# Kernel optimization log

Hardware: AMD Instinct MI355X
Metric: run time of the kernel (lower is better)

The kernel has to match this reference:

```python
import jax, jax.numpy as jnp
import numpy as np

B, T, D, H, TW = 4, 2048, 2048, 8, 4
DH = D // H


def setup_inputs() -> dict:
    key = jax.random.key(0)
    ks = jax.random.split(key, 16)
    s = lambda k, shape, std: jax.random.normal(k, shape, dtype=jnp.float32) * std
    inp = {
        "x": jax.random.normal(ks[0], (B, T, D), dtype=jnp.float32),
        "segment_pos": jnp.tile(jnp.arange(T, dtype=jnp.int32), (B, 1)),
        # linear_y / linear_x: width -> lru_width, std = 1/sqrt(width)
        "Wy": s(ks[1], (D, D), (1.0 / D) ** 0.5),
        "by": jnp.zeros((D,), jnp.float32),
        "Wx": s(ks[2], (D, D), (1.0 / D) ** 0.5),
        "bx": jnp.zeros((D,), jnp.float32),
        # depthwise causal conv: [temporal_width, lru_width]
        "conv_w": s(ks[3], (TW, D), (1.0 / TW) ** 0.5),
        "conv_b": jnp.zeros((D,), jnp.float32),
        # RG-LRU block-diagonal gates: [H, D/H, D/H]
        "gx_w": s(ks[4], (H, DH, DH), (1.0 / DH) ** 0.5),
        "gx_b": jnp.zeros((H, DH), jnp.float32),
        "ga_w": s(ks[5], (H, DH, DH), (1.0 / DH) ** 0.5),
        "ga_b": jnp.zeros((H, DH), jnp.float32),
        # a_param: softplus(a_param) > 0 controls decay rate
        "a_param": jnp.log(jnp.exp(jax.random.uniform(ks[6], (D,), minval=0.3, maxval=0.9)) - 1.0 + 1e-6),
        # linear_out: lru_width -> width, std = 1/sqrt(lru_width)
        "Wout": s(ks[7], (D, D), (1.0 / D) ** 0.5),
        "bout": jnp.zeros((D,), jnp.float32),
    }
    return inp


def _causal_conv1d(x, w, b, segment_pos):
    # depthwise causal conv over time; contributions from other segments masked
    t = x.shape[1]
    acc = jnp.zeros_like(x)
    for i in range(TW):
        shift = TW - 1 - i  # input at t - shift, weighted by w[i]
        xs = x if shift == 0 else jnp.pad(x, ((0, 0), (shift, 0), (0, 0)))[:, :t]
        mask = (segment_pos >= shift)[..., None].astype(x.dtype)
        acc = acc + xs * mask * w[i]
    return acc + b


def _rg_lru(x, segment_pos, gx_w, gx_b, ga_w, ga_b, a_param):
    b, t, d = x.shape
    xr = x.reshape(b, t, H, DH)
    gate_x = jax.nn.sigmoid(jnp.einsum("bthi,hij->bthj", xr, gx_w) + gx_b).reshape(b, t, d)
    gate_a = jax.nn.sigmoid(jnp.einsum("bthi,hij->bthj", xr, ga_w) + ga_b).reshape(b, t, d)
    log_a = -8.0 * gate_a * jax.nn.softplus(a_param)  # [B,T,D]
    a = jnp.exp(log_a)
    reset = (segment_pos == 0)[..., None]  # [B,T,1]
    multiplier = jnp.sqrt(jnp.maximum(1.0 - jnp.exp(2.0 * log_a), 0.0))
    multiplier = jnp.where(reset, 1.0, multiplier)
    normed = x * gate_x * multiplier
    a_scan = jnp.where(reset, 0.0, a)

    def step(h, inputs):
        a_t, x_t = inputs
        h = a_t * h + x_t
        return h, h

    h0 = jnp.zeros((b, d), x.dtype)
    _, ys = jax.lax.scan(step, h0, (a_scan.transpose(1, 0, 2), normed.transpose(1, 0, 2)))
    return ys.transpose(1, 0, 2)


def reference(x, segment_pos, Wy, by, Wx, bx, conv_w, conv_b, gx_w, gx_b, ga_w, ga_b, a_param, Wout, bout):
    y = jax.nn.gelu(x @ Wy.T + by, approximate=True)
    x_proj = x @ Wx.T + bx
    x_conv = _causal_conv1d(x_proj, conv_w, conv_b, segment_pos)
    x_lru = _rg_lru(x_conv, segment_pos, gx_w, gx_b, ga_w, ga_b, a_param)
    out = (x_lru * y) @ Wout.T + bout
    return out
```

## Files before the change

kernel.cpp:

```cpp
#include <hip/hip_runtime.h>
#include <cstdint>
#include <cstddef>

typedef __bf16 bf16;
typedef __bf16 bf16x8 __attribute__((ext_vector_type(8)));
typedef __bf16 bf16x4 __attribute__((ext_vector_type(4)));
typedef float f32x4 __attribute__((ext_vector_type(4)));

#define BDIM 4
#define TDIM 2048
#define DDIM 2048
#define HDIM 8
#define DHD 256
#define MTOT 8192
#define NCHUNK 64
#define LCHUNK 32

__device__ __forceinline__ void stage16(const bf16* g, bf16* l) {
  __builtin_amdgcn_global_load_lds(
      (const __attribute__((address_space(1))) void*)g,
      (__attribute__((address_space(3))) void*)l, 16, 0, 0);
}

#define BARX() __builtin_amdgcn_s_barrier()
#define SCHB() __builtin_amdgcn_sched_barrier(0)
#define WAITVM(N) asm volatile("s_waitcnt vmcnt(" #N ")")

__device__ __forceinline__ float sigmoid_f(float x) {
  return __fdividef(1.f, 1.f + __expf(-x));
}
__device__ __forceinline__ float gelu_tanh(float v) {
  float u = 0.7978845608028654f * (v + 0.044715f * v * v * v);
  u = fminf(fmaxf(u, -15.f), 15.f);
  float t = __expf(2.f * u);
  return 0.5f * v * (1.f + __fdividef(t - 1.f, t + 1.f));
}
__device__ __forceinline__ float softplus_f(float x) {
  return __logf(1.f + __expf(x));
}

__global__ __launch_bounds__(256) void f2b(const float* __restrict__ src,
                                           bf16* __restrict__ dst) {
  size_t i = ((size_t)blockIdx.x * 256 + threadIdx.x) * 8;
  const float4 a = *(const float4*)(src + i);
  const float4 b = *(const float4*)(src + i + 4);
  bf16x8 r;
  r[0] = (bf16)a.x; r[1] = (bf16)a.y; r[2] = (bf16)a.z; r[3] = (bf16)a.w;
  r[4] = (bf16)b.x; r[5] = (bf16)b.y; r[6] = (bf16)b.z; r[7] = (bf16)b.w;
  *(bf16x8*)(dst + i) = r;
}

__global__ __launch_bounds__(256) void f2b2(const float* __restrict__ s0,
                                            const float* __restrict__ s1,
                                            bf16* __restrict__ d0,
                                            bf16* __restrict__ d1) {
  const float* src = blockIdx.y ? s1 : s0;
  bf16* dst = blockIdx.y ? d1 : d0;
  size_t i = ((size_t)blockIdx.x * 256 + threadIdx.x) * 8;
  const float4 a = *(const float4*)(src + i);
  const float4 b = *(const float4*)(src + i + 4);
  bf16x8 r;
  r[0] = (bf16)a.x; r[1] = (bf16)a.y; r[2] = (bf16)a.z; r[3] = (bf16)a.w;
  r[4] = (bf16)b.x; r[5] = (bf16)b.y; r[6] = (bf16)b.z; r[7] = (bf16)b.w;
  *(bf16x8*)(dst + i) = r;
}

template <typename TO, int EPI>
__global__ __launch_bounds__(512, 2) void gemm256(
    const bf16* __restrict__ A, const bf16* __restrict__ Bm,
    const float* __restrict__ bias, TO* __restrict__ C,
    int K, int lda, int ldb, int ldc) {
  const int gx = gridDim.x, gy = gridDim.y;
  const int nwg = gx * gy;
  const int did = blockIdx.x + gx * blockIdx.y;
  const int cpx = nwg >> 3;
  const int lid = (did & 7) * cpx + (did >> 3);
  const int n0 = (lid % gx) * 256;
  const int m0 = (lid / gx) * 256;

  __shared__ bf16 sA0[256 * 64];
  __shared__ bf16 sA1[256 * 64];
  __shared__ bf16 sB0[256 * 64];
  __shared__ bf16 sB1[256 * 64];
  const int tid = threadIdx.x;
  const int lane = tid & 63;
  const int wid = tid >> 6;
  const int wr = wid >> 2;
  const int wc = wid & 3;
  const int quad = lane >> 4;
  const int l15 = lane & 15;

  const int sr = tid >> 3;
  const int ks8 = ((tid & 7) ^ (sr & 7)) << 3;
  const bf16* Ag = A + (size_t)(m0 + sr) * lda + ks8;
  const bf16* Bg = Bm + (size_t)(n0 + sr) * ldb + ks8;

  const int swz0 = ((quad) ^ (l15 & 7)) << 3;
  const int swz1 = ((4 + quad) ^ (l15 & 7)) << 3;

  f32x4 acc[8][4];
#pragma unroll
  for (int i = 0; i < 8; ++i)
#pragma unroll
    for (int j = 0; j < 4; ++j)
#pragma unroll
      for (int r = 0; r < 4; ++r) acc[i][j][r] = 0.f;

  const int NT = K >> 6;

#define STG_A(ARR, H, TK)                                                     \
  do {                                                                        \
    _Pragma("unroll") for (int j_ = 0; j_ < 2; ++j_) {                        \
      const int c_ = (H) * 2 + j_;                                            \
      stage16(Ag + (size_t)(c_ * 64) * lda + (size_t)(TK) * 64,               \
              &ARR[(c_ * 64 + wid * 8) * 64]);                                \
    }                                                                         \
  } while (0)
#define STG_B(ARR, H, TK)                                                     \
  do {                                                                        \
    _Pragma("unroll") for (int j_ = 0; j_ < 2; ++j_) {                        \
      const int c_ = (H) * 2 + j_;                                            \
      stage16(Bg + (size_t)(c_ * 64) * ldb + (size_t)(TK) * 64,               \
              &ARR[(c_ * 64 + wid * 8) * 64]);                                \
    }                                                                         \
  } while (0)

  bf16x8 aq0[4][2], aq1[4][2], b0[2][2], b1[2][2];

#define RDA(DST, MH, ARR)                                                     \
  do {                                                                        \
    _Pragma("unroll") for (int mi_ = 0; mi_ < 4; ++mi_) {                     \
      const int arow_ = wr * 128 + (MH) * 64 + mi_ * 16 + l15;                \
      DST[mi_][0] = *(const bf16x8*)(&ARR[arow_ * 64] + swz0);                \
      DST[mi_][1] = *(const bf16x8*)(&ARR[arow_ * 64] + swz1);                \
    }                                                                         \
  } while (0)
#define RDB(DST, NH, ARR)                                                     \
  do {                                                                        \
    _Pragma("unroll") for (int ni_ = 0; ni_ < 2; ++ni_) {                     \
      const int brow_ = wc * 64 + (NH) * 32 + ni_ * 16 + l15;                 \
      DST[ni_][0] = *(const bf16x8*)(&ARR[brow_ * 64] + swz0);                \
      DST[ni_][1] = *(const bf16x8*)(&ARR[brow_ * 64] + swz1);                \
    }                                                                         \
  } while (0)
#define MFMAQ(MH, NH, AA, BB)                                                 \
  do {                                                                        \
    __builtin_amdgcn_s_setprio(1);                                            \
    _Pragma("unroll") for (int mi_ = 0; mi_ < 4; ++mi_)                       \
        _Pragma("unroll") for (int ni_ = 0; ni_ < 2; ++ni_) {                 \
      acc[(MH)*4 + mi_][(NH)*2 + ni_] = __builtin_amdgcn_mfma_f32_16x16x32_bf16( \
          AA[mi_][0], BB[ni_][0], acc[(MH)*4 + mi_][(NH)*2 + ni_], 0, 0, 0);  \
      acc[(MH)*4 + mi_][(NH)*2 + ni_] = __builtin_amdgcn_mfma_f32_16x16x32_bf16( \
          AA[mi_][1], BB[ni_][1], acc[(MH)*4 + mi_][(NH)*2 + ni_], 0, 0, 0);  \
    }                                                                         \
    __builtin_amdgcn_s_setprio(0);                                            \
  } while (0)

#define TILE(SAs, SBs, SAo, SBo, T)                                           \
  do {                                                                        \
    const int tn_ = ((T) + 1 < NT) ? (T) + 1 : NT - 1;                        \
    const int tnn_ = ((T) + 2 < NT) ? (T) + 2 : NT - 1;                       \
                                                                     \
    WAITVM(4);                                                                \
    SCHB();                                                                   \
    STG_B(SBo, 1, tn_);                                                       \
    RDB(b1, 1, SBs);                                                          \
    MFMAQ(0, 0, aq0, b0);                                                     \
    BARX();                                                                   \
                                                                     \
    STG_A(SAo, 1, tn_);                                                       \
    RDA(aq1, 1, SAs);                                                         \
    MFMAQ(0, 1, aq0, b1);                                                     \
    BARX();                                                                   \
                                                                     \
    STG_B(SBs, 0, tnn_);                                                      \
    MFMAQ(1, 0, aq1, b0);                                                     \
    BARX();                                                                   \
                                                                     \
    WAITVM(6);                                                                \
    SCHB();                                                                   \
    if (T + 1 < NT) {                                                         \
      RDA(aq0, 0, SAo);                                                       \
      RDB(b0, 0, SBo);                                                        \
    }                                                                         \
    STG_A(SAs, 0, tnn_);                                                      \
    MFMAQ(1, 1, aq1, b1);                                                     \
    BARX();                                                                   \
  } while (0)

  STG_B(sB0, 0, 0); STG_A(sA0, 0, 0);
  STG_B(sB0, 1, 0); STG_A(sA0, 1, 0);
  STG_B(sB1, 0, 1); STG_A(sA1, 0, 1);
  WAITVM(8);
  SCHB();
  BARX();
  RDA(aq0, 0, sA0);
  RDB(b0, 0, sB0);

  for (int t = 0; t < NT; t += 2) {
    TILE(sA0, sB0, sA1, sB1, t);
    TILE(sA1, sB1, sA0, sB0, t + 1);
  }
  WAITVM(0);

#undef STG_A
#undef STG_B
#undef RDA
#undef RDB
#undef MFMAQ
#undef TILE

  float bv[4];
#pragma unroll
  for (int nn = 0; nn < 4; ++nn) bv[nn] = bias[n0 + wc * 64 + nn * 16 + l15];
#pragma unroll
  for (int mm = 0; mm < 8; ++mm) {
#pragma unroll
    for (int r = 0; r < 4; ++r) {
      const int m = m0 + wr * 128 + mm * 16 + quad * 4 + r;
      TO* Crow = C + (size_t)m * ldc + n0 + wc * 64 + l15;
#pragma unroll
      for (int nn = 0; nn < 4; ++nn) {
        float v = acc[mm][nn][r] + bv[nn];
        if (EPI == 1) v = gelu_tanh(v);
        Crow[nn * 16] = (TO)v;
      }
    }
  }
}

template <typename TO>
__global__ __launch_bounds__(256, 2) void gemm128(
    const bf16* __restrict__ A,
    const bf16* __restrict__ B0m, const bf16* __restrict__ B1m,
    const float* __restrict__ bias0, const float* __restrict__ bias1,
    TO* __restrict__ C0, TO* __restrict__ C1, int epi1,
    int K, int lda, int ldb, int ldc) {
  const bf16* Bm = blockIdx.z ? B1m : B0m;
  const float* bias = blockIdx.z ? bias1 : bias0;
  TO* C = blockIdx.z ? C1 : C0;
  const int EPI = blockIdx.z ? epi1 : 0;

  const int gx = gridDim.x, gy = gridDim.y;
  const int nwg = gx * gy;
  const int did = blockIdx.x + gx * blockIdx.y;
  const int cpx = nwg >> 3;
  const int lid = (did & 7) * cpx + (did >> 3);
  const int n0 = (lid % gx) * 128;
  const int m0 = (lid / gx) * 128;

  __shared__ bf16 sA0[128 * 64];
  __shared__ bf16 sA1[128 * 64];
  __shared__ bf16 sB0[128 * 64];
  __shared__ bf16 sB1[128 * 64];
  const int tid = threadIdx.x;
  const int lane = tid & 63;
  const int wid = tid >> 6;
  const int wr = wid >> 1;
  const int wc = wid & 1;
  const int quad = lane >> 4;
  const int l15 = lane & 15;

  const int sr = tid >> 3;
  const int ks8 = ((tid & 7) ^ (sr & 7)) << 3;
  const bf16* Ag = A + (size_t)(m0 + sr) * lda + ks8;
  const bf16* Bg = Bm + (size_t)(n0 + sr) * ldb + ks8;

  const int swz0 = ((quad) ^ (l15 & 7)) << 3;
  const int swz1 = ((4 + quad) ^ (l15 & 7)) << 3;

  f32x4 acc[4][4];
#pragma unroll
  for (int i = 0; i < 4; ++i)
#pragma unroll
    for (int j = 0; j < 4; ++j)
#pragma unroll
      for (int r = 0; r < 4; ++r) acc[i][j][r] = 0.f;

  const int NT = K >> 6;

#define STG_A(ARR, TK)                                                        \
  do {                                                                        \
    _Pragma("unroll") for (int c_ = 0; c_ < 4; ++c_)                          \
        stage16(Ag + (size_t)(c_ * 32) * lda + (size_t)(TK) * 64,             \
                &ARR[(c_ * 32 + wid * 8) * 64]);                              \
  } while (0)
#define STG_B(ARR, TK)                                                        \
  do {                                                                        \
    _Pragma("unroll") for (int c_ = 0; c_ < 4; ++c_)                          \
        stage16(Bg + (size_t)(c_ * 32) * ldb + (size_t)(TK) * 64,             \
                &ARR[(c_ * 32 + wid * 8) * 64]);                              \
  } while (0)

  bf16x8 af[4][2], b0[2][2], b1[2][2];

#define RDA(ARR)                                                              \
  do {                                                                        \
    _Pragma("unroll") for (int mi_ = 0; mi_ < 4; ++mi_) {                     \
      const int arow_ = wr * 64 + mi_ * 16 + l15;                             \
      af[mi_][0] = *(const bf16x8*)(&ARR[arow_ * 64] + swz0);                 \
      af[mi_][1] = *(const bf16x8*)(&ARR[arow_ * 64] + swz1);                 \
    }                                                                         \
  } while (0)
#define RDB(DST, NH, ARR)                                                     \
  do {                                                                        \
    _Pragma("unroll") for (int ni_ = 0; ni_ < 2; ++ni_) {                     \
      const int brow_ = wc * 64 + (NH) * 32 + ni_ * 16 + l15;                 \
      DST[ni_][0] = *(const bf16x8*)(&ARR[brow_ * 64] + swz0);                \
      DST[ni_][1] = *(const bf16x8*)(&ARR[brow_ * 64] + swz1);                \
    }                                                                         \
  } while (0)
#define MFMAQ(NH, BB)                                                         \
  do {                                                                        \
    __builtin_amdgcn_s_setprio(1);                                            \
    _Pragma("unroll") for (int mi_ = 0; mi_ < 4; ++mi_)                       \
        _Pragma("unroll") for (int ni_ = 0; ni_ < 2; ++ni_) {                 \
      acc[mi_][(NH)*2 + ni_] = __builtin_amdgcn_mfma_f32_16x16x32_bf16(       \
          af[mi_][0], BB[ni_][0], acc[mi_][(NH)*2 + ni_], 0, 0, 0);           \
      acc[mi_][(NH)*2 + ni_] = __builtin_amdgcn_mfma_f32_16x16x32_bf16(       \
          af[mi_][1], BB[ni_][1], acc[mi_][(NH)*2 + ni_], 0, 0, 0);           \
    }                                                                         \
    __builtin_amdgcn_s_setprio(0);                                            \
  } while (0)

#define TILE(SAs, SBs, SAo, SBo, T)                                           \
  do {                                                                        \
    const int tn_ = ((T) + 1 < NT) ? (T) + 1 : NT - 1;                        \
    const int tnn_ = ((T) + 2 < NT) ? (T) + 2 : NT - 1;                       \
                                                                     \
    RDA(SAs);                                                                 \
    RDB(b0, 0, SBs);                                                          \
    STG_B(SBo, tn_);                                                          \
    MFMAQ(0, b0);                                                             \
    BARX();                                                                   \
                                                                     \
    RDB(b1, 1, SBs);                                                          \
    STG_A(SAs, tnn_);                                                         \
    MFMAQ(1, b1);                                                             \
    WAITVM(4);                                                                \
    BARX();                                                                   \
  } while (0)

  const int t1 = (NT > 1) ? 1 : 0;
  STG_B(sB0, 0); STG_A(sA0, 0);
  STG_B(sB1, t1); STG_A(sA1, t1);
  WAITVM(4);
  SCHB();
  BARX();

  for (int t = 0; t < NT; t += 2) {
    TILE(sA0, sB0, sA1, sB1, t);
    TILE(sA1, sB1, sA0, sB0, t + 1);
  }
  WAITVM(0);

#undef STG_A
#undef STG_B
#undef RDA
#undef RDB
#undef MFMAQ
#undef TILE

  float bv[4];
#pragma unroll
  for (int nn = 0; nn < 4; ++nn) bv[nn] = bias[n0 + wc * 64 + nn * 16 + l15];
#pragma unroll
  for (int mm = 0; mm < 4; ++mm) {
#pragma unroll
    for (int r = 0; r < 4; ++r) {
      const int m = m0 + wr * 64 + mm * 16 + quad * 4 + r;
      TO* Crow = C + (size_t)m * ldc + n0 + wc * 64 + l15;
#pragma unroll
      for (int nn = 0; nn < 4; ++nn) {
        float v = acc[mm][nn][r] + bv[nn];
        if (EPI == 1) v = gelu_tanh(v);
        Crow[nn * 16] = (TO)v;
      }
    }
  }
}

__global__ __launch_bounds__(256) void gate_gemm(
    const bf16* __restrict__ xconv,
    const bf16* __restrict__ gxT, const bf16* __restrict__ gaT,
    bf16* __restrict__ gxr, bf16* __restrict__ gar) {
  const int h = blockIdx.z >> 1;
  const int g = blockIdx.z & 1;
  const bf16* A = xconv + h * DHD;
  const bf16* Bm = (g ? gaT : gxT) + (size_t)h * DHD * DHD;
  bf16* C = (g ? gar : gxr) + h * DHD;
  const int n0 = blockIdx.x * 128;
  const int m0 = blockIdx.y * 128;
  __shared__ bf16 As[128 * 32];
  __shared__ bf16 Bs[128 * 32];
  const int tid = threadIdx.x;
  const int lane = tid & 63;
  const int wid = tid >> 6;
  const int waveM = wid >> 1, waveN = wid & 1;
  const int quad = lane >> 4;
  const int l15 = lane & 15;
  const int srow = lane >> 2;
  const int scol = (lane & 3) * 8;

  f32x4 acc[4][4];
#pragma unroll
  for (int i = 0; i < 4; ++i)
#pragma unroll
    for (int j = 0; j < 4; ++j)
#pragma unroll
      for (int r = 0; r < 4; ++r) acc[i][j][r] = 0.f;

  for (int k0 = 0; k0 < DHD; k0 += 32) {
    if (k0) __syncthreads();
#pragma unroll
    for (int cc = 0; cc < 2; ++cc) {
      const int q = wid * 2 + cc;
      const int row = q * 16 + srow;
      stage16(A + (size_t)(m0 + row) * DDIM + k0 + scol, As + q * 512);
      stage16(Bm + (size_t)(n0 + row) * DHD + k0 + scol, Bs + q * 512);
    }
    __syncthreads();
    bf16x8 af[4], bfr[4];
#pragma unroll
    for (int i = 0; i < 4; ++i) {
      af[i]  = *(const bf16x8*)&As[(waveM * 64 + i * 16 + l15) * 32 + quad * 8];
      bfr[i] = *(const bf16x8*)&Bs[(waveN * 64 + i * 16 + l15) * 32 + quad * 8];
    }
#pragma unroll
    for (int i = 0; i < 4; ++i)
#pragma unroll
      for (int j = 0; j < 4; ++j)
        acc[i][j] = __builtin_amdgcn_mfma_f32_16x16x32_bf16(af[i], bfr[j], acc[i][j], 0, 0, 0);
  }

#pragma unroll
  for (int j = 0; j < 4; ++j) {
    const int n = n0 + waveN * 64 + j * 16 + l15;
#pragma unroll
    for (int i = 0; i < 4; ++i) {
#pragma unroll
      for (int r = 0; r < 4; ++r) {
        const int m = m0 + waveM * 64 + i * 16 + quad * 4 + r;
        C[(size_t)m * DDIM + n] = (bf16)acc[i][j][r];
      }
    }
  }
}

__global__ __launch_bounds__(256) void conv_kernel(
    const bf16* __restrict__ xp, const float* __restrict__ cw,
    const float* __restrict__ cb, const int* __restrict__ segp,
    bf16* __restrict__ xc) {
  int v = blockIdx.x * 256 + threadIdx.x;
  int dv = v & (DDIM / 8 - 1);
  int m = v >> 8;
  int d0 = dv * 8;
  int t = m & (TDIM - 1);
  int sp = segp[m];
  float acc[8];
#pragma unroll
  for (int j = 0; j < 8; ++j) acc[j] = cb[d0 + j];
#pragma unroll
  for (int i = 0; i < 4; ++i) {
    int shift = 3 - i;
    if (t >= shift && sp >= shift) {
      bf16x8 xv = *(const bf16x8*)&xp[(size_t)(m - shift) * DDIM + d0];
#pragma unroll
      for (int j = 0; j < 8; ++j) acc[j] = fmaf((float)xv[j], cw[i * DDIM + d0 + j], acc[j]);
    }
  }
  bf16x8 o;
#pragma unroll
  for (int j = 0; j < 8; ++j) o[j] = (bf16)acc[j];
  *(bf16x8*)&xc[(size_t)m * DDIM + d0] = o;
}

__global__ __launch_bounds__(256) void transpose_gates(
    const float* __restrict__ gxw, const float* __restrict__ gaw,
    bf16* __restrict__ gxT, bf16* __restrict__ gaT) {
  __shared__ bf16 tile[32][33];
  int zz = blockIdx.z;
  int h = zz >> 1;
  const float* src = (zz & 1) ? gaw : gxw;
  bf16* dst = (zz & 1) ? gaT : gxT;
  int j0 = blockIdx.x * 32;
  int i0 = blockIdx.y * 32;
  int r = threadIdx.x >> 5;
  int c = threadIdx.x & 31;
  for (int rr = r; rr < 32; rr += 8)
    tile[rr][c] = (bf16)src[(size_t)(h * DHD + i0 + rr) * DHD + j0 + c];
  __syncthreads();
  for (int rr = r; rr < 32; rr += 8)
    dst[(size_t)(h * DHD + j0 + rr) * DHD + i0 + c] = tile[c][rr];
}

__device__ __forceinline__ void lru_elem(float pgx, float pga, float xc,
                                         float spv, bool reset,
                                         float& a, float& nr) {
  const float gx = sigmoid_f(pgx);
  const float ga = sigmoid_f(pga);
  const float la = -8.f * ga * spv;
  a = reset ? 0.f : __expf(la);
  const float mult = reset ? 1.f : sqrtf(fmaxf(1.f - __expf(2.f * la), 0.f));
  nr = xc * gx * mult;
}

__global__ __launch_bounds__(256) void scan_phase1(
    const bf16* __restrict__ gxr, const bf16* __restrict__ gar,
    const bf16* __restrict__ xconv,
    const float* __restrict__ gxb, const float* __restrict__ gab,
    const float* __restrict__ apar, const int* __restrict__ segp,
    float* __restrict__ chA, float* __restrict__ chH) {
  int idx = blockIdx.x * 256 + threadIdx.x;
  int dv = idx & (DDIM / 4 - 1);
  int c = (idx >> 9) & (NCHUNK - 1);
  int b = idx >> 15;
  int d0 = dv * 4;
  const float4 gx4 = *(const float4*)(gxb + d0);
  const float4 ga4 = *(const float4*)(gab + d0);
  const float4 ap4 = *(const float4*)(apar + d0);
  float gxbv[4] = {gx4.x, gx4.y, gx4.z, gx4.w};
  float gabv[4] = {ga4.x, ga4.y, ga4.z, ga4.w};
  float spv[4]  = {softplus_f(ap4.x), softplus_f(ap4.y),
                   softplus_f(ap4.z), softplus_f(ap4.w)};
  const int mrow = b * TDIM + c * LCHUNK;
  size_t base = (size_t)mrow * DDIM + d0;
  float A[4] = {1.f, 1.f, 1.f, 1.f}, hh[4] = {0.f, 0.f, 0.f, 0.f};
  for (int i = 0; i < LCHUNK; ++i) {
    size_t o = base + (size_t)i * DDIM;
    bf16x4 g1 = *(const bf16x4*)&gxr[o];
    bf16x4 g2 = *(const bf16x4*)&gar[o];
    bf16x4 xv = *(const bf16x4*)&xconv[o];
    bool rst = (segp[mrow + i] == 0);
#pragma unroll
    for (int j = 0; j < 4; ++j) {
      float a, nr;
      lru_elem((float)g1[j] + gxbv[j], (float)g2[j] + gabv[j], (float)xv[j],
               spv[j], rst, a, nr);
      hh[j] = fmaf(a, hh[j], nr);
      A[j] *= a;
    }
  }
  size_t ci = (size_t)(b * NCHUNK + c) * DDIM + d0;
  *(f32x4*)&chA[ci] = f32x4{A[0], A[1], A[2], A[3]};
  *(f32x4*)&chH[ci] = f32x4{hh[0], hh[1], hh[2], hh[3]};
}

__global__ __launch_bounds__(256) void scan_phase2(
    const float* __restrict__ chA, const float* __restrict__ chH,
    float* __restrict__ hst) {
  int idx = blockIdx.x * 64 + threadIdx.x;
  int d = idx & (DDIM - 1);
  int b = idx >> 11;
  float s = 0.f;
  for (int c = 0; c < NCHUNK; ++c) {
    int ci = (b * NCHUNK + c) * DDIM + d;
    hst[ci] = s;
    s = fmaf(chA[ci], s, chH[ci]);
  }
}

__global__ __launch_bounds__(256) void scan_phase3(
    const bf16* __restrict__ gxr, const bf16* __restrict__ gar,
    const bf16* __restrict__ xconv,
    const float* __restrict__ gxb, const float* __restrict__ gab,
    const float* __restrict__ apar, const int* __restrict__ segp,
    const float* __restrict__ hst, bf16* __restrict__ yz) {
  int idx = blockIdx.x * 256 + threadIdx.x;
  int dv = idx & (DDIM / 4 - 1);
  int c = (idx >> 9) & (NCHUNK - 1);
  int b = idx >> 15;
  int d0 = dv * 4;
  const float4 gx4 = *(const float4*)(gxb + d0);
  const float4 ga4 = *(const float4*)(gab + d0);
  const float4 ap4 = *(const float4*)(apar + d0);
  float gxbv[4] = {gx4.x, gx4.y, gx4.z, gx4.w};
  float gabv[4] = {ga4.x, ga4.y, ga4.z, ga4.w};
  float spv[4]  = {softplus_f(ap4.x), softplus_f(ap4.y),
                   softplus_f(ap4.z), softplus_f(ap4.w)};
  const int mrow = b * TDIM + c * LCHUNK;
  size_t base = (size_t)mrow * DDIM + d0;
  size_t ci = (size_t)(b * NCHUNK + c) * DDIM + d0;
  const float4 h4 = *(const float4*)(hst + ci);
  float hh[4] = {h4.x, h4.y, h4.z, h4.w};
  for (int i = 0; i < LCHUNK; ++i) {
    size_t o = base + (size_t)i * DDIM;
    bf16x4 g1 = *(const bf16x4*)&gxr[o];
    bf16x4 g2 = *(const bf16x4*)&gar[o];
    bf16x4 xv = *(const bf16x4*)&xconv[o];
    bf16x4 y4 = *(const bf16x4*)&yz[o];
    bool rst = (segp[mrow + i] == 0);
    bf16x4 out;
#pragma unroll
    for (int j = 0; j < 4; ++j) {
      float a, nr;
      lru_elem((float)g1[j] + gxbv[j], (float)g2[j] + gabv[j], (float)xv[j],
               spv[j], rst, a, nr);
      hh[j] = fmaf(a, hh[j], nr);
      out[j] = (bf16)(hh[j] * (float)y4[j]);
    }
    *(bf16x4*)&yz[o] = out;
  }
}

extern "C" void kernel_launch(void* const* d_in, const int* in_sizes, int n_in,
                              void* d_out, int out_size, void* d_ws, size_t ws_size,
                              hipStream_t stream) {
  const float* x    = (const float*)d_in[0];
  const int*   segp = (const int*)d_in[1];
  const float* Wy   = (const float*)d_in[2];
  const float* by   = (const float*)d_in[3];
  const float* Wx   = (const float*)d_in[4];
  const float* bx   = (const float*)d_in[5];
  const float* cw   = (const float*)d_in[6];
  const float* cb   = (const float*)d_in[7];
  const float* gxw  = (const float*)d_in[8];
  const float* gxb  = (const float*)d_in[9];
  const float* gaw  = (const float*)d_in[10];
  const float* gab  = (const float*)d_in[11];
  const float* apar = (const float*)d_in[12];
  const float* Wout = (const float*)d_in[13];
  const float* bout = (const float*)d_in[14];

  const size_t MD = (size_t)MTOT * DDIM;
  const size_t WD = (size_t)DDIM * DDIM;
  bf16* xb    = (bf16*)d_out;
  bf16* xproj = (bf16*)((char*)d_out + MD * 2);
  bf16* xconv = xb;
  bf16* gxr   = xproj;

  char* ws = (char*)d_ws;
  bf16*  gar = (bf16*)ws;
  bf16*  W1  = (bf16*)(ws + MD * 2);
  bf16*  WB1 = (bf16*)(ws + 2 * MD * 2);
  bf16*  WB2 = (bf16*)(ws + 2 * MD * 2 + WD * 2);
  char*  tail = ws + 2 * MD * 2 + 2 * WD * 2;
  const size_t GW = (size_t)HDIM * DHD * DHD * 2;
  const size_t CH = (size_t)BDIM * NCHUNK * DDIM * 4;
  bf16*  gxT = (bf16*)tail;
  bf16*  gaT = (bf16*)(tail + GW);
  float* chA = (float*)(tail + 2 * GW);
  float* chH = (float*)(tail + 2 * GW + CH);
  float* hst = (float*)(tail + 2 * GW + 2 * CH);

  dim3 blk(256);
  f2b<<<dim3(MD / 2048), blk, 0, stream>>>(x, xb);
  f2b2<<<dim3(WD / 2048, 2), blk, 0, stream>>>(Wx, Wy, WB1, WB2);
  transpose_gates<<<dim3(8, 8, 16), blk, 0, stream>>>(gxw, gaw, gxT, gaT);

  gemm128<bf16><<<dim3(16, 64, 2), blk, 0, stream>>>(
      xb, WB1, WB2, bx, by, xproj, W1, 1, DDIM, DDIM, DDIM, DDIM);

  conv_kernel<<<dim3(MTOT * (DDIM / 8) / 256), blk, 0, stream>>>(xproj, cw, cb, segp, xconv);

  gate_gemm<<<dim3(2, 64, 16), blk, 0, stream>>>(xconv, gxT, gaT, gxr, gar);

  scan_phase1<<<dim3(BDIM * NCHUNK * (DDIM / 4) / 256), blk, 0, stream>>>(
      gxr, gar, xconv, gxb, gab, apar, segp, chA, chH);
  scan_phase2<<<dim3(BDIM * DDIM / 64), dim3(64), 0, stream>>>(chA, chH, hst);
  scan_phase3<<<dim3(BDIM * NCHUNK * (DDIM / 4) / 256), blk, 0, stream>>>(
      gxr, gar, xconv, gxb, gab, apar, segp, hst, W1);

  f2b<<<dim3(WD / 2048), blk, 0, stream>>>(Wout, WB1);
  gemm256<float, 0><<<dim3(8, 32), dim3(512), 0, stream>>>(
      W1, WB1, bout, (float*)d_out, DDIM, DDIM, DDIM, DDIM);
}
```

Baseline: 416.6 us.

## Pipeline gate GEMM with swizzled double-buffered LDS and merge conversion launches

Rewrites the block-diagonal gate GEMM to use 64-wide K tiles with double-buffered, XOR-swizzled LDS staging. Loads are interleaved with MFMA issue under raised priority, and workgroup IDs are remapped for cache locality. It also fuses the x/Wx/Wy fp32→bf16 conversions into one launch and folds the Wout conversion into the conv kernel's extra blocks, removing launches. This adds code complexity and relies on WB1 no longer being needed once the projection GEMM has finished.

```diff
diff --git a/kernel.cpp b/kernel.cpp
--- a/kernel.cpp
+++ b/kernel.cpp
@@ -39,9 +39,9 @@
   return __logf(1.f + __expf(x));
 }
 
-__global__ __launch_bounds__(256) void f2b(const float* __restrict__ src,
-                                           bf16* __restrict__ dst) {
-  size_t i = ((size_t)blockIdx.x * 256 + threadIdx.x) * 8;
+__device__ __forceinline__ void f2b_body(const float* __restrict__ src,
+                                         bf16* __restrict__ dst, int vb) {
+  size_t i = ((size_t)vb * 256 + threadIdx.x) * 8;
   const float4 a = *(const float4*)(src + i);
   const float4 b = *(const float4*)(src + i + 4);
   bf16x8 r;
@@ -50,19 +50,14 @@
   *(bf16x8*)(dst + i) = r;
 }
 
-__global__ __launch_bounds__(256) void f2b2(const float* __restrict__ s0,
-                                            const float* __restrict__ s1,
-                                            bf16* __restrict__ d0,
-                                            bf16* __restrict__ d1) {
-  const float* src = blockIdx.y ? s1 : s0;
-  bf16* dst = blockIdx.y ? d1 : d0;
-  size_t i = ((size_t)blockIdx.x * 256 + threadIdx.x) * 8;
-  const float4 a = *(const float4*)(src + i);
-  const float4 b = *(const float4*)(src + i + 4);
-  bf16x8 r;
-  r[0] = (bf16)a.x; r[1] = (bf16)a.y; r[2] = (bf16)a.z; r[3] = (bf16)a.w;
-  r[4] = (bf16)b.x; r[5] = (bf16)b.y; r[6] = (bf16)b.z; r[7] = (bf16)b.w;
-  *(bf16x8*)(dst + i) = r;
+__global__ __launch_bounds__(256) void f2b3(
+    const float* __restrict__ x, bf16* __restrict__ xb,
+    const float* __restrict__ Wx, bf16* __restrict__ WB1,
+    const float* __restrict__ Wy, bf16* __restrict__ WB2) {
+  int b = blockIdx.x;
+  if (b < 8192)       f2b_body(x, xb, b);
+  else if (b < 10240) f2b_body(Wx, WB1, b - 8192);
+  else                f2b_body(Wy, WB2, b - 10240);
 }
 
 template <typename TO, int EPI>
@@ -380,7 +375,7 @@
   }
 }
 
-__global__ __launch_bounds__(256) void gate_gemm(
+__global__ __launch_bounds__(256, 2) void gate128(
     const bf16* __restrict__ xconv,
     const bf16* __restrict__ gxT, const bf16* __restrict__ gaT,
     bf16* __restrict__ gxr, bf16* __restrict__ gar) {
@@ -389,18 +384,34 @@
   const bf16* A = xconv + h * DHD;
   const bf16* Bm = (g ? gaT : gxT) + (size_t)h * DHD * DHD;
   bf16* C = (g ? gar : gxr) + h * DHD;
-  const int n0 = blockIdx.x * 128;
-  const int m0 = blockIdx.y * 128;
-  __shared__ bf16 As[128 * 32];
-  __shared__ bf16 Bs[128 * 32];
+
+  const int gx = gridDim.x, gy = gridDim.y;
+  const int nwg = gx * gy;
+  const int did = blockIdx.x + gx * blockIdx.y;
+  const int cpx = nwg >> 3;
+  const int lid = (did & 7) * cpx + (did >> 3);
+  const int n0 = (lid % gx) * 128;
+  const int m0 = (lid / gx) * 128;
+
+  __shared__ bf16 sA0[128 * 64];
+  __shared__ bf16 sA1[128 * 64];
+  __shared__ bf16 sB0[128 * 64];
+  __shared__ bf16 sB1[128 * 64];
   const int tid = threadIdx.x;
   const int lane = tid & 63;
   const int wid = tid >> 6;
-  const int waveM = wid >> 1, waveN = wid & 1;
+  const int wr = wid >> 1;
+  const int wc = wid & 1;
   const int quad = lane >> 4;
   const int l15 = lane & 15;
-  const int srow = lane >> 2;
-  const int scol = (lane & 3) * 8;
+
+  const int sr = tid >> 3;
+  const int ks8 = ((tid & 7) ^ (sr & 7)) << 3;
+  const bf16* Ag = A + (size_t)(m0 + sr) * DDIM + ks8;
+  const bf16* Bg = Bm + (size_t)(n0 + sr) * DHD + ks8;
+
+  const int swz0 = ((quad) ^ (l15 & 7)) << 3;
+  const int swz1 = ((4 + quad) ^ (l15 & 7)) << 3;
 
   f32x4 acc[4][4];
 #pragma unroll
@@ -410,39 +421,96 @@
 #pragma unroll
       for (int r = 0; r < 4; ++r) acc[i][j][r] = 0.f;
 
-  for (int k0 = 0; k0 < DHD; k0 += 32) {
-    if (k0) __syncthreads();
-#pragma unroll
-    for (int cc = 0; cc < 2; ++cc) {
-      const int q = wid * 2 + cc;
-      const int row = q * 16 + srow;
-      stage16(A + (size_t)(m0 + row) * DDIM + k0 + scol, As + q * 512);
-      stage16(Bm + (size_t)(n0 + row) * DHD + k0 + scol, Bs + q * 512);
-    }
-    __syncthreads();
-    bf16x8 af[4], bfr[4];
-#pragma unroll
-    for (int i = 0; i < 4; ++i) {
-      af[i]  = *(const bf16x8*)&As[(waveM * 64 + i * 16 + l15) * 32 + quad * 8];
-      bfr[i] = *(const bf16x8*)&Bs[(waveN * 64 + i * 16 + l15) * 32 + quad * 8];
-    }
-#pragma unroll
-    for (int i = 0; i < 4; ++i)
-#pragma unroll
-      for (int j = 0; j < 4; ++j)
-        acc[i][j] = __builtin_amdgcn_mfma_f32_16x16x32_bf16(af[i], bfr[j], acc[i][j], 0, 0, 0);
-  }
-
-#pragma unroll
-  for (int j = 0; j < 4; ++j) {
-    const int n = n0 + waveN * 64 + j * 16 + l15;
-#pragma unroll
-    for (int i = 0; i < 4; ++i) {
-#pragma unroll
-      for (int r = 0; r < 4; ++r) {
-        const int m = m0 + waveM * 64 + i * 16 + quad * 4 + r;
-        C[(size_t)m * DDIM + n] = (bf16)acc[i][j][r];
-      }
+  const int NT = 4;
+
+#define STG_A(ARR, TK)                                                        \
+  do {                                                                        \
+    _Pragma("unroll") for (int c_ = 0; c_ < 4; ++c_)                          \
+        stage16(Ag + (size_t)(c_ * 32) * DDIM + (size_t)(TK) * 64,            \
+                &ARR[(c_ * 32 + wid * 8) * 64]);                              \
+  } while (0)
+#define STG_B(ARR, TK)                                                        \
+  do {                                                                        \
+    _Pragma("unroll") for (int c_ = 0; c_ < 4; ++c_)                          \
+        stage16(Bg + (size_t)(c_ * 32) * DHD + (size_t)(TK) * 64,             \
+                &ARR[(c_ * 32 + wid * 8) * 64]);                              \
+  } while (0)
+
+  bf16x8 af[4][2], b0[2][2], b1[2][2];
+
+#define RDA(ARR)                                                              \
+  do {                                                                        \
+    _Pragma("unroll") for (int mi_ = 0; mi_ < 4; ++mi_) {                     \
+      const int arow_ = wr * 64 + mi_ * 16 + l15;                             \
+      af[mi_][0] = *(const bf16x8*)(&ARR[arow_ * 64] + swz0);                 \
+      af[mi_][1] = *(const bf16x8*)(&ARR[arow_ * 64] + swz1);                 \
+    }                                                                         \
+  } while (0)
+#define RDB(DST, NH, ARR)                                                     \
+  do {                                                                        \
+    _Pragma("unroll") for (int ni_ = 0; ni_ < 2; ++ni_) {                     \
+      const int brow_ = wc * 64 + (NH) * 32 + ni_ * 16 + l15;                 \
+      DST[ni_][0] = *(const bf16x8*)(&ARR[brow_ * 64] + swz0);                \
+      DST[ni_][1] = *(const bf16x8*)(&ARR[brow_ * 64] + swz1);                \
+    }                                                                         \
+  } while (0)
+#define MFMAQ(NH, BB)                                                         \
+  do {                                                                        \
+    __builtin_amdgcn_s_setprio(1);                                            \
+    _Pragma("unroll") for (int mi_ = 0; mi_ < 4; ++mi_)                       \
+        _Pragma("unroll") for (int ni_ = 0; ni_ < 2; ++ni_) {                 \
+      acc[mi_][(NH)*2 + ni_] = __builtin_amdgcn_mfma_f32_16x16x32_bf16(       \
+          af[mi_][0], BB[ni_][0], acc[mi_][(NH)*2 + ni_], 0, 0, 0);           \
+      acc[mi_][(NH)*2 + ni_] = __builtin_amdgcn_mfma_f32_16x16x32_bf16(       \
+          af[mi_][1], BB[ni_][1], acc[mi_][(NH)*2 + ni_], 0, 0, 0);           \
+    }                                                                         \
+    __builtin_amdgcn_s_setprio(0);                                            \
+  } while (0)
+
+#define TILE(SAs, SBs, SAo, SBo, T)                                           \
+  do {                                                                        \
+    const int tn_ = ((T) + 1 < NT) ? (T) + 1 : NT - 1;                        \
+    const int tnn_ = ((T) + 2 < NT) ? (T) + 2 : NT - 1;                       \
+    RDA(SAs);                                                                 \
+    RDB(b0, 0, SBs);                                                          \
+    STG_B(SBo, tn_);                                                          \
+    MFMAQ(0, b0);                                                             \
+    BARX();                                                                   \
+    RDB(b1, 1, SBs);                                                          \
+    STG_A(SAs, tnn_);                                                         \
+    MFMAQ(1, b1);                                                             \
+    WAITVM(4);                                                                \
+    BARX();                                                                   \
+  } while (0)
+
+  STG_B(sB0, 0); STG_A(sA0, 0);
+  STG_B(sB1, 1); STG_A(sA1, 1);
+  WAITVM(4);
+  SCHB();
+  BARX();
+
+  for (int t = 0; t < NT; t += 2) {
+    TILE(sA0, sB0, sA1, sB1, t);
+    TILE(sA1, sB1, sA0, sB0, t + 1);
+  }
+  WAITVM(0);
+
+#undef STG_A
+#undef STG_B
+#undef RDA
+#undef RDB
+#undef MFMAQ
+#undef TILE
+
+#pragma unroll
+  for (int mm = 0; mm < 4; ++mm) {
+#pragma unroll
+    for (int r = 0; r < 4; ++r) {
+      const int m = m0 + wr * 64 + mm * 16 + quad * 4 + r;
+      bf16* Crow = C + (size_t)m * DDIM + n0 + wc * 64 + l15;
+#pragma unroll
+      for (int nn = 0; nn < 4; ++nn)
+        Crow[nn * 16] = (bf16)acc[mm][nn][r];
     }
   }
 }
@@ -450,7 +518,12 @@
 __global__ __launch_bounds__(256) void conv_kernel(
     const bf16* __restrict__ xp, const float* __restrict__ cw,
     const float* __restrict__ cb, const int* __restrict__ segp,
-    bf16* __restrict__ xc) {
+    bf16* __restrict__ xc,
+    const float* __restrict__ Wout, bf16* __restrict__ WB1) {
+  if (blockIdx.x >= 8192) {
+    f2b_body(Wout, WB1, blockIdx.x - 8192);
+    return;
+  }
   int v = blockIdx.x * 256 + threadIdx.x;
   int dv = v & (DDIM / 8 - 1);
   int m = v >> 8;
@@ -644,16 +717,16 @@
   float* hst = (float*)(tail + 2 * GW + 2 * CH);
 
   dim3 blk(256);
-  f2b<<<dim3(MD / 2048), blk, 0, stream>>>(x, xb);
-  f2b2<<<dim3(WD / 2048, 2), blk, 0, stream>>>(Wx, Wy, WB1, WB2);
+  f2b3<<<dim3(12288), blk, 0, stream>>>(x, xb, Wx, WB1, Wy, WB2);
   transpose_gates<<<dim3(8, 8, 16), blk, 0, stream>>>(gxw, gaw, gxT, gaT);
 
   gemm128<bf16><<<dim3(16, 64, 2), blk, 0, stream>>>(
       xb, WB1, WB2, bx, by, xproj, W1, 1, DDIM, DDIM, DDIM, DDIM);
 
-  conv_kernel<<<dim3(MTOT * (DDIM / 8) / 256), blk, 0, stream>>>(xproj, cw, cb, segp, xconv);
-
-  gate_gemm<<<dim3(2, 64, 16), blk, 0, stream>>>(xconv, gxT, gaT, gxr, gar);
+  conv_kernel<<<dim3(8192 + 2048), blk, 0, stream>>>(
+      xproj, cw, cb, segp, xconv, Wout, WB1);
+
+  gate128<<<dim3(2, 64, 16), blk, 0, stream>>>(xconv, gxT, gaT, gxr, gar);
 
   scan_phase1<<<dim3(BDIM * NCHUNK * (DDIM / 4) / 256), blk, 0, stream>>>(
       gxr, gar, xconv, gxb, gab, apar, segp, chA, chH);
@@ -661,7 +734,6 @@
   scan_phase3<<<dim3(BDIM * NCHUNK * (DDIM / 4) / 256), blk, 0, stream>>>(
       gxr, gar, xconv, gxb, gab, apar, segp, hst, W1);
 
-  f2b<<<dim3(WD / 2048), blk, 0, stream>>>(Wout, WB1);
   gemm256<float, 0><<<dim3(8, 32), dim3(512), 0, stream>>>(
       W1, WB1, bout, (float*)d_out, DDIM, DDIM, DDIM, DDIM);
 }
```

Measured after the change: 412.5 us. No clear change (-1.0%).
